# Kernel optimization log

Hardware: AMD Instinct MI355X
Metric: run time of the kernel (lower is better)

## Reference

```python
import jax, jax.numpy as jnp
import numpy as np

NOISE_DIM = 32
HIDDEN_DIM = 256
DATA_DIM = 2
TEMP = 0.05
N = 16384
DIAG_PENALTY = 1e6


def _cdist(a, b):
    # Euclidean pairwise distance [Na, Nb], safe sqrt (zero grad at d==0 like torch.cdist)
    d2 = (jnp.sum(a * a, -1)[:, None] + jnp.sum(b * b, -1)[None, :]
          - 2.0 * (a @ b.T))
    d2 = jnp.maximum(d2, 0.0)
    safe = jnp.where(d2 > 0, d2, 1.0)
    return jnp.where(d2 > 0, jnp.sqrt(safe), 0.0)


def setup_inputs() -> dict:
    key = jax.random.key(0)
    ks = jax.random.split(key, 12)
    pos = jax.random.normal(ks[0], (N, DATA_DIM), dtype=jnp.float32)
    z = jax.random.normal(ks[1], (N, NOISE_DIM), dtype=jnp.float32)
    def lin(k, fan_in, fan_out):
        bound = 1.0 / np.sqrt(fan_in)
        k1, k2 = jax.random.split(k)
        W = jax.random.uniform(k1, (fan_in, fan_out), minval=-bound, maxval=bound, dtype=jnp.float32)
        b = jax.random.uniform(k2, (fan_out,), minval=-bound, maxval=bound, dtype=jnp.float32)
        return W, b
    W1, b1 = lin(ks[2], NOISE_DIM, HIDDEN_DIM)
    W2, b2 = lin(ks[3], HIDDEN_DIM, HIDDEN_DIM)
    W3, b3 = lin(ks[4], HIDDEN_DIM, HIDDEN_DIM)
    W4, b4 = lin(ks[5], HIDDEN_DIM, HIDDEN_DIM)
    W5, b5 = lin(ks[6], HIDDEN_DIM, DATA_DIM)
    return {"pos": pos, "z": z, "W1": W1, "b1": b1, "W2": W2, "b2": b2,
            "W3": W3, "b3": b3, "W4": W4, "b4": b4, "W5": W5, "b5": b5}


def reference(pos, z, W1, b1, W2, b2, W3, b3, W4, b4, W5, b5):
    # SELU MLP generator
    h = jax.nn.selu(z @ W1 + b1)
    h = jax.nn.selu(h @ W2 + b2)
    h = jax.nn.selu(h @ W3 + b3)
    h = jax.nn.selu(h @ W4 + b4)
    gen = h @ W5 + b5  # [N, D]

    y_pos = jax.lax.stop_gradient(pos)
    y_neg = jax.lax.stop_gradient(gen)

    dist_pos = _cdist(gen, y_pos)  # [N, N]
    dist_neg = _cdist(gen, y_neg)  # [N, N]
    dist_neg = dist_neg + jnp.eye(gen.shape[0], dtype=gen.dtype) * DIAG_PENALTY

    energy_pos = -TEMP * jax.nn.logsumexp(-dist_pos / TEMP, axis=1)
    energy_neg = TEMP * jax.nn.logsumexp(-dist_neg / TEMP, axis=1)
    return energy_pos + energy_neg  # [N]
```

## Files before the change

### kernel.cpp

```cpp
#include <hip/hip_runtime.h>
#include <hip/hip_bf16.h>

#define N_PTS 16384
#define TEMP_F 0.05f

__device__ __forceinline__ float selu_f(float x) {
    const float scale = 1.0507009873554805f;
    const float alpha = 1.6732632423543772f;
    return x > 0.f ? scale * x : scale * alpha * (__expf(x) - 1.f);
}

__device__ __forceinline__ float fast_sqrtf(float x) {
#if __has_builtin(__builtin_amdgcn_sqrtf)
    return __builtin_amdgcn_sqrtf(x);
#else
    return sqrtf(x);
#endif
}

__device__ __forceinline__ float fast_exp2f(float x) {
#if __has_builtin(__builtin_amdgcn_exp2f)
    return __builtin_amdgcn_exp2f(x);
#else
    return exp2f(x);
#endif
}

__device__ __forceinline__ float fast_log2f(float x) {
#if __has_builtin(__builtin_amdgcn_logf)
    return __builtin_amdgcn_logf(x);
#else
    return log2f(x);
#endif
}

__global__ __launch_bounds__(1024) void mlp_kernel(
    const float* __restrict__ z,
    const float* __restrict__ W1, const float* __restrict__ b1,
    const float* __restrict__ W2, const float* __restrict__ b2,
    const float* __restrict__ W3, const float* __restrict__ b3,
    const float* __restrict__ W4, const float* __restrict__ b4,
    const float* __restrict__ W5, const float* __restrict__ b5,
    float* __restrict__ gen)
{
    __shared__ float h[256 * 64];

    const int t = threadIdx.x;
    const int r = t & 63;
    const int w = __builtin_amdgcn_readfirstlane(t >> 6);
    const int c0 = w * 16;
    const int row0 = blockIdx.x * 64;

    #pragma unroll
    for (int e = 0; e < 2; e++) {
        int f  = t + e * 1024;
        int rz = f >> 5;
        int kz = f & 31;
        h[kz * 64 + rz] = z[(row0 + rz) * 32 + kz];
    }
    __syncthreads();

    float acc[16];

    #pragma unroll
    for (int j = 0; j < 16; j++) acc[j] = b1[c0 + j];
    #pragma unroll 8
    for (int k = 0; k < 32; k++) {
        float hv = h[k * 64 + r];
        const float* Wr = W1 + k * 256 + c0;
        #pragma unroll
        for (int j = 0; j < 16; j++) acc[j] = fmaf(hv, Wr[j], acc[j]);
    }
    __syncthreads();
    #pragma unroll
    for (int j = 0; j < 16; j++) h[(c0 + j) * 64 + r] = selu_f(acc[j]);
    __syncthreads();

    for (int layer = 0; layer < 3; layer++) {
        const float* W = (layer == 0) ? W2 : (layer == 1) ? W3 : W4;
        const float* b = (layer == 0) ? b2 : (layer == 1) ? b3 : b4;
        #pragma unroll
        for (int j = 0; j < 16; j++) acc[j] = b[c0 + j];
        #pragma unroll 4
        for (int k = 0; k < 256; k++) {
            float hv = h[k * 64 + r];
            const float* Wr = W + k * 256 + c0;
            #pragma unroll
            for (int j = 0; j < 16; j++) acc[j] = fmaf(hv, Wr[j], acc[j]);
        }
        __syncthreads();
        #pragma unroll
        for (int j = 0; j < 16; j++) h[(c0 + j) * 64 + r] = selu_f(acc[j]);
        __syncthreads();
    }

    float p0 = 0.f, p1 = 0.f;
    #pragma unroll
    for (int kk = 0; kk < 16; kk++) {
        int k = c0 + kk;
        float hv = h[k * 64 + r];
        p0 = fmaf(hv, W5[k * 2 + 0], p0);
        p1 = fmaf(hv, W5[k * 2 + 1], p1);
    }
    __syncthreads();
    h[(0 * 16 + w) * 64 + r] = p0;
    h[(1 * 16 + w) * 64 + r] = p1;
    __syncthreads();
    if (t < 128) {
        int d  = t >> 6;
        int rr = t & 63;
        float sum = b5[d];
        #pragma unroll
        for (int ss = 0; ss < 16; ss++) sum += h[(d * 16 + ss) * 64 + rr];
        gen[(row0 + rr) * 2 + d] = sum;
    }
}

__global__ __launch_bounds__(512) void energy_kernel(
    const float* __restrict__ gen,
    const float* __restrict__ pos,
    float* __restrict__ out)
{
    __shared__ float4 sp[512];
    __shared__ float4 sg[512];

    const int t  = threadIdx.x;
    const int s  = t & 31;
    const int rl = t >> 5;
    const int i  = blockIdx.x * 16 + rl;
    const int diagBase = ((blockIdx.x * 16) >> 10) << 10;

    const float2 q = ((const float2*)gen)[i];

    const float cL2 = 28.853900817779268f;
    const float Tl2 = 0.034657359027997264f;
    const float cB  = 57.707801635558536f;

    float p0 = 0.f, p1 = 0.f, n0 = 0.f, n1 = 0.f;

    for (int base = 0; base < N_PTS; base += 1024) {
        __syncthreads();
        sp[t] = ((const float4*)pos)[base / 2 + t];
        sg[t] = ((const float4*)gen)[base / 2 + t];
        __syncthreads();
        if (base == diagBase) {
            #pragma unroll 4
            for (int u = 0; u < 16; u++) {
                int j = base + 2 * (s + 32 * u);
                float4 pp = sp[s + 32 * u];
                float4 gg = sg[s + 32 * u];
                float dx = q.x - pp.x, dy = q.y - pp.y;
                float d  = fast_sqrtf(fmaf(dx, dx, dy * dy));
                p0 += fast_exp2f(fmaf(-cL2, d, cB));
                dx = q.x - pp.z; dy = q.y - pp.w;
                d  = fast_sqrtf(fmaf(dx, dx, dy * dy));
                p1 += fast_exp2f(fmaf(-cL2, d, cB));
                dx = q.x - gg.x; dy = q.y - gg.y;
                d  = fast_sqrtf(fmaf(dx, dx, dy * dy));
                float e0 = fast_exp2f(fmaf(-cL2, d, cB));
                n0 += (j == i) ? 0.f : e0;
                dx = q.x - gg.z; dy = q.y - gg.w;
                d  = fast_sqrtf(fmaf(dx, dx, dy * dy));
                float e1 = fast_exp2f(fmaf(-cL2, d, cB));
                n1 += (j + 1 == i) ? 0.f : e1;
            }
        } else {
            #pragma unroll 4
            for (int u = 0; u < 16; u++) {
                float4 pp = sp[s + 32 * u];
                float4 gg = sg[s + 32 * u];
                float dx = q.x - pp.x, dy = q.y - pp.y;
                float d  = fast_sqrtf(fmaf(dx, dx, dy * dy));
                p0 += fast_exp2f(fmaf(-cL2, d, cB));
                dx = q.x - pp.z; dy = q.y - pp.w;
                d  = fast_sqrtf(fmaf(dx, dx, dy * dy));
                p1 += fast_exp2f(fmaf(-cL2, d, cB));
                dx = q.x - gg.x; dy = q.y - gg.y;
                d  = fast_sqrtf(fmaf(dx, dx, dy * dy));
                n0 += fast_exp2f(fmaf(-cL2, d, cB));
                dx = q.x - gg.z; dy = q.y - gg.w;
                d  = fast_sqrtf(fmaf(dx, dx, dy * dy));
                n1 += fast_exp2f(fmaf(-cL2, d, cB));
            }
        }
    }

    float sump = p0 + p1;
    float sumn = n0 + n1;
    #pragma unroll
    for (int m = 1; m < 32; m <<= 1) {
        sump += __shfl_xor(sump, m, 32);
        sumn += __shfl_xor(sumn, m, 32);
    }

    if (s == 0) {
        out[i] = Tl2 * (fast_log2f(sumn) - fast_log2f(sump));
    }
}

extern "C" void kernel_launch(void* const* d_in, const int* in_sizes, int n_in,
                              void* d_out, int out_size, void* d_ws, size_t ws_size,
                              hipStream_t stream) {
    const float* pos = (const float*)d_in[0];
    const float* z   = (const float*)d_in[1];
    const float* W1  = (const float*)d_in[2];
    const float* b1  = (const float*)d_in[3];
    const float* W2  = (const float*)d_in[4];
    const float* b2  = (const float*)d_in[5];
    const float* W3  = (const float*)d_in[6];
    const float* b3  = (const float*)d_in[7];
    const float* W4  = (const float*)d_in[8];
    const float* b4  = (const float*)d_in[9];
    const float* W5  = (const float*)d_in[10];
    const float* b5  = (const float*)d_in[11];

    float* gen = (float*)d_ws;

    mlp_kernel<<<N_PTS / 64, 1024, 0, stream>>>(z, W1, b1, W2, b2, W3, b3,
                                                W4, b4, W5, b5, gen);
    energy_kernel<<<N_PTS / 16, 512, 0, stream>>>(gen, pos, (float*)d_out);
}
```

Before: 292.9 us.

## Register-tile MLP kernel and double-buffer weight tiles through shared memory

The MLP kernel is rebuilt to use 32-row blocks of 512 threads, where each thread accumulates a 4-row by 4-column register tile instead of one row by 16 columns. Weight tiles for the hidden layers are staged in shared memory with double buffering: the next tile's global load is issued while the current tile is being used. This aims to cut redundant global weight reads and raise the amount of arithmetic per shared-memory load. In exchange it uses more shared memory per block, launches twice as many blocks and adds a barrier per 16-row weight tile. The energy kernel is unchanged.

```diff
diff --git a/kernel.cpp b/kernel.cpp
--- a/kernel.cpp
+++ b/kernel.cpp
@@ -34,7 +34,9 @@
 #endif
 }
 
-__global__ __launch_bounds__(1024) void mlp_kernel(
+#define HS 36
+
+__global__ __launch_bounds__(512) void mlp_kernel(
     const float* __restrict__ z,
     const float* __restrict__ W1, const float* __restrict__ b1,
     const float* __restrict__ W2, const float* __restrict__ b2,
@@ -43,76 +45,142 @@
     const float* __restrict__ W5, const float* __restrict__ b5,
     float* __restrict__ gen)
 {
-    __shared__ float h[256 * 64];
-
-    const int t = threadIdx.x;
-    const int r = t & 63;
-    const int w = __builtin_amdgcn_readfirstlane(t >> 6);
-    const int c0 = w * 16;
-    const int row0 = blockIdx.x * 64;
+    __shared__ float hbuf[256 * HS];
+    __shared__ float wbuf[2][16 * 256];
+
+    const int t  = threadIdx.x;
+    const int l  = t & 63;
+    const int w  = t >> 6;
+    const int r0 = w * 4;
+    const int row0 = blockIdx.x * 32;
 
     #pragma unroll
     for (int e = 0; e < 2; e++) {
-        int f  = t + e * 1024;
+        int f  = t + e * 512;
         int rz = f >> 5;
         int kz = f & 31;
-        h[kz * 64 + rz] = z[(row0 + rz) * 32 + kz];
+        hbuf[kz * HS + rz] = z[(row0 + rz) * 32 + kz];
+    }
+    float* wflat = &wbuf[0][0];
+    #pragma unroll
+    for (int e = 0; e < 4; e++) {
+        int f = t + e * 512;
+        ((float4*)wflat)[f] = ((const float4*)W1)[f];
     }
     __syncthreads();
 
-    float acc[16];
-
-    #pragma unroll
-    for (int j = 0; j < 16; j++) acc[j] = b1[c0 + j];
-    #pragma unroll 8
+    float2 acc[4][2];
+
+    #pragma unroll
+    for (int g = 0; g < 2; g++) {
+        float2 bv = *(const float2*)&b1[2 * l + 128 * g];
+        #pragma unroll
+        for (int i = 0; i < 4; i++) acc[i][g] = bv;
+    }
+    #pragma unroll 4
     for (int k = 0; k < 32; k++) {
-        float hv = h[k * 64 + r];
-        const float* Wr = W1 + k * 256 + c0;
-        #pragma unroll
-        for (int j = 0; j < 16; j++) acc[j] = fmaf(hv, Wr[j], acc[j]);
+        float hv[4];
+        float2 wv[2];
+        *(float4*)&hv[0] = *(const float4*)&hbuf[k * HS + r0];
+        #pragma unroll
+        for (int g = 0; g < 2; g++)
+            wv[g] = *(const float2*)&wflat[k * 256 + 2 * l + 128 * g];
+        #pragma unroll
+        for (int i = 0; i < 4; i++)
+            #pragma unroll
+            for (int g = 0; g < 2; g++) {
+                acc[i][g].x = fmaf(hv[i], wv[g].x, acc[i][g].x);
+                acc[i][g].y = fmaf(hv[i], wv[g].y, acc[i][g].y);
+            }
     }
     __syncthreads();
     #pragma unroll
-    for (int j = 0; j < 16; j++) h[(c0 + j) * 64 + r] = selu_f(acc[j]);
-    __syncthreads();
+    for (int i = 0; i < 4; i++)
+        #pragma unroll
+        for (int g = 0; g < 2; g++) {
+            int c = 2 * l + 128 * g;
+            hbuf[c * HS + r0 + i]       = selu_f(acc[i][g].x);
+            hbuf[(c + 1) * HS + r0 + i] = selu_f(acc[i][g].y);
+        }
 
     for (int layer = 0; layer < 3; layer++) {
         const float* W = (layer == 0) ? W2 : (layer == 1) ? W3 : W4;
         const float* b = (layer == 0) ? b2 : (layer == 1) ? b3 : b4;
         #pragma unroll
-        for (int j = 0; j < 16; j++) acc[j] = b[c0 + j];
+        for (int g = 0; g < 2; g++) {
+            float2 bv = *(const float2*)&b[2 * l + 128 * g];
+            #pragma unroll
+            for (int i = 0; i < 4; i++) acc[i][g] = bv;
+        }
+        ((float4*)&wbuf[0][0])[t]       = ((const float4*)W)[t];
+        ((float4*)&wbuf[0][0])[t + 512] = ((const float4*)W)[t + 512];
+        __syncthreads();
+
+        for (int s = 0; s < 16; s++) {
+            const int buf = s & 1;
+            float4 nx0, nx1;
+            if (s + 1 < 16) {
+                nx0 = ((const float4*)W)[(s + 1) * 1024 + t];
+                nx1 = ((const float4*)W)[(s + 1) * 1024 + t + 512];
+            }
+            const float* wl = &wbuf[buf][0];
+            #pragma unroll 4
+            for (int kk = 0; kk < 16; kk++) {
+                const int k = s * 16 + kk;
+                float hv[4];
+                float2 wv[2];
+                *(float4*)&hv[0] = *(const float4*)&hbuf[k * HS + r0];
+                #pragma unroll
+                for (int g = 0; g < 2; g++)
+                    wv[g] = *(const float2*)&wl[kk * 256 + 2 * l + 128 * g];
+                #pragma unroll
+                for (int i = 0; i < 4; i++)
+                    #pragma unroll
+                    for (int g = 0; g < 2; g++) {
+                        acc[i][g].x = fmaf(hv[i], wv[g].x, acc[i][g].x);
+                        acc[i][g].y = fmaf(hv[i], wv[g].y, acc[i][g].y);
+                    }
+            }
+            if (s + 1 < 16) {
+                ((float4*)&wbuf[1 - buf][0])[t]       = nx0;
+                ((float4*)&wbuf[1 - buf][0])[t + 512] = nx1;
+            }
+            __syncthreads();
+        }
+        #pragma unroll
+        for (int i = 0; i < 4; i++)
+            #pragma unroll
+            for (int g = 0; g < 2; g++) {
+                int c = 2 * l + 128 * g;
+                hbuf[c * HS + r0 + i]       = selu_f(acc[i][g].x);
+                hbuf[(c + 1) * HS + r0 + i] = selu_f(acc[i][g].y);
+            }
+        if (layer == 2) __syncthreads();
+    }
+
+    {
+        const int slot = t >> 5;
+        const int rr   = t & 31;
+        float p0 = 0.f, p1 = 0.f;
         #pragma unroll 4
-        for (int k = 0; k < 256; k++) {
-            float hv = h[k * 64 + r];
-            const float* Wr = W + k * 256 + c0;
-            #pragma unroll
-            for (int j = 0; j < 16; j++) acc[j] = fmaf(hv, Wr[j], acc[j]);
-        }
-        __syncthreads();
-        #pragma unroll
-        for (int j = 0; j < 16; j++) h[(c0 + j) * 64 + r] = selu_f(acc[j]);
-        __syncthreads();
-    }
-
-    float p0 = 0.f, p1 = 0.f;
-    #pragma unroll
-    for (int kk = 0; kk < 16; kk++) {
-        int k = c0 + kk;
-        float hv = h[k * 64 + r];
-        p0 = fmaf(hv, W5[k * 2 + 0], p0);
-        p1 = fmaf(hv, W5[k * 2 + 1], p1);
-    }
-    __syncthreads();
-    h[(0 * 16 + w) * 64 + r] = p0;
-    h[(1 * 16 + w) * 64 + r] = p1;
-    __syncthreads();
-    if (t < 128) {
-        int d  = t >> 6;
-        int rr = t & 63;
-        float sum = b5[d];
-        #pragma unroll
-        for (int ss = 0; ss < 16; ss++) sum += h[(d * 16 + ss) * 64 + rr];
-        gen[(row0 + rr) * 2 + d] = sum;
+        for (int kk = 0; kk < 16; kk++) {
+            int k = slot * 16 + kk;
+            float hv = hbuf[k * HS + rr];
+            float2 w5 = *(const float2*)&W5[2 * k];
+            p0 = fmaf(hv, w5.x, p0);
+            p1 = fmaf(hv, w5.y, p1);
+        }
+        wbuf[0][slot * 32 + rr]       = p0;
+        wbuf[0][512 + slot * 32 + rr] = p1;
+        __syncthreads();
+        if (t < 64) {
+            int d = t >> 5;
+            int r = t & 31;
+            float sum = b5[d];
+            #pragma unroll
+            for (int ss = 0; ss < 16; ss++) sum += wbuf[0][d * 512 + ss * 32 + r];
+            gen[(row0 + r) * 2 + d] = sum;
+        }
     }
 }
 
@@ -216,7 +284,7 @@
 
     float* gen = (float*)d_ws;
 
-    mlp_kernel<<<N_PTS / 64, 1024, 0, stream>>>(z, W1, b1, W2, b2, W3, b3,
-                                                W4, b4, W5, b5, gen);
+    mlp_kernel<<<N_PTS / 32, 512, 0, stream>>>(z, W1, b1, W2, b2, W3, b3,
+                                               W4, b4, W5, b5, gen);
     energy_kernel<<<N_PTS / 16, 512, 0, stream>>>(gen, pos, (float*)d_out);
 }
```

Result: slower. 304.9 us (+4.1%).
